# Kernel optimization log

Hardware: AMD Instinct MI355X
Metric: run time of the kernel (lower is better)

The kernel has to match this reference:

```python
import jax, jax.numpy as jnp
import numpy as np

B, T, V, H = 256, 512, 64, 256
IN = 2 * V + 1  # values + masks + delta_t = 129


def setup_inputs() -> dict:
    key = jax.random.key(0)
    ks = jax.random.split(key, 8)
    # sorted positive times with some entries zeroed (ragged padding -> t_exist False)
    t = jnp.sort(jax.random.uniform(ks[0], (B, T)), axis=1)
    keep = jax.random.uniform(ks[1], (B, T)) < 0.9
    times_in = jnp.where(keep, t, 0.0).astype(jnp.float32)
    data_in = jax.random.normal(ks[2], (B, T, V), dtype=jnp.float32)
    mask_in = (jax.random.uniform(ks[3], (B, T, V)) < 0.8).astype(jnp.float32)
    s = 1.0 / np.sqrt(H).astype(np.float32)
    W_ih = jax.random.uniform(ks[4], (3 * H, IN), minval=-s, maxval=s, dtype=jnp.float32)
    W_hh = jax.random.uniform(ks[5], (3 * H, H), minval=-s, maxval=s, dtype=jnp.float32)
    b_ih = jax.random.uniform(ks[6], (3 * H,), minval=-s, maxval=s, dtype=jnp.float32)
    b_hh = jax.random.uniform(ks[7], (3 * H,), minval=-s, maxval=s, dtype=jnp.float32)
    return {"times_in": times_in, "data_in": data_in, "mask_in": mask_in,
            "W_ih": W_ih, "W_hh": W_hh, "b_ih": b_ih, "b_hh": b_hh}


def reference(times_in, data_in, mask_in, W_ih, W_hh, b_ih, b_hh):
    b = times_in.shape[0]
    # delta_ts: times[:,1:] - times[:,:-1], padded with zero at the end
    delta = jnp.concatenate(
        [times_in[:, 1:] - times_in[:, :-1],
         jnp.zeros((b, 1), times_in.dtype)], axis=1)  # [B,T]
    # input_series = cat(values, masks, delta_t) -> [B,T,2V+1]
    x = jnp.concatenate([data_in, mask_in, delta[..., None]], axis=-1)
    t_exist = times_in > 0  # [B,T]
    h0 = jnp.zeros((b, W_hh.shape[1]), x.dtype)

    xs = (jnp.swapaxes(x, 0, 1), jnp.swapaxes(t_exist, 0, 1))  # time-major

    def step(h, inp):
        xt, m = inp  # xt: [B,IN], m: [B]
        gx = xt @ W_ih.T + b_ih  # [B,3H]
        gh = h @ W_hh.T + b_hh   # [B,3H]
        xr, xz, xn = jnp.split(gx, 3, axis=-1)
        hr, hz, hn = jnp.split(gh, 3, axis=-1)
        r = jax.nn.sigmoid(xr + hr)
        z = jax.nn.sigmoid(xz + hz)
        n = jnp.tanh(xn + r * hn)
        h_new = (1.0 - z) * n + z * h
        h = jnp.where(m[:, None], h_new, h)  # masked state carry
        return h, None

    h_final, _ = jax.lax.scan(step, h0, xs)
    return h_final
```

## Files before the change

kernel.cpp:

```cpp
#include <hip/hip_runtime.h>

#define Bn 256
#define Tn 512
#define Vn 64
#define Hn 256
#define INn 129
#define Cc 8
#define NCH (Tn / Cc)
#define WU 68
#define WSZ (768 * WU)
#define GX_OFF (262144)
#define GX_BYTES ((size_t)Bn * Tn * 768 * 2)
#define AST 168
#define CST 264

typedef __fp16 half2_t __attribute__((ext_vector_type(2)));
typedef __fp16 half8_t __attribute__((ext_vector_type(8)));
typedef float f32x4 __attribute__((ext_vector_type(4)));

static __device__ __forceinline__ unsigned int cvt2(float a, float b) {
  return __builtin_bit_cast(unsigned int, __builtin_amdgcn_cvt_pkrtz(a, b));
}

static __device__ __forceinline__ float dot2(unsigned int w, unsigned int x, float acc) {
#if __has_builtin(__builtin_amdgcn_fdot2)
  return __builtin_amdgcn_fdot2(__builtin_bit_cast(half2_t, w),
                                __builtin_bit_cast(half2_t, x), acc, false);
#else
  half2_t a = __builtin_bit_cast(half2_t, w);
  half2_t b = __builtin_bit_cast(half2_t, x);
  return acc + (float)a.x * (float)b.x + (float)a.y * (float)b.y;
#endif
}

static __device__ __forceinline__ float pair_sum(float v) {
#if __has_builtin(__builtin_amdgcn_update_dpp)
  int x = __builtin_amdgcn_update_dpp(0, __builtin_bit_cast(int, v), 0xB1, 0xF, 0xF, true);
  return v + __builtin_bit_cast(float, x);
#else
  int j = __builtin_amdgcn_ds_swizzle(__builtin_bit_cast(int, v), 0x041F);
  return v + __builtin_bit_cast(float, j);
#endif
}

static __device__ __forceinline__ float fast_exp2(float x) {
#if __has_builtin(__builtin_amdgcn_exp2f)
  return __builtin_amdgcn_exp2f(x);
#else
  return exp2f(x);
#endif
}
static __device__ __forceinline__ float fast_rcp(float x) {
#if __has_builtin(__builtin_amdgcn_rcpf)
  return __builtin_amdgcn_rcpf(x);
#else
  return 1.f / x;
#endif
}
static __device__ __forceinline__ float sigmoid_f(float x) {
  return fast_rcp(1.f + fast_exp2(-1.44269504f * x));
}
static __device__ __forceinline__ float tanh_f(float x) {
  return 1.f - 2.f * fast_rcp(1.f + fast_exp2(2.88539008f * x));
}
static __device__ __forceinline__ float h2f(unsigned short u) {
  return (float)__builtin_bit_cast(__fp16, u);
}

__global__ void convert_wih(const float* __restrict__ W_ih, unsigned int* __restrict__ w16) {
  int idx = blockIdx.x * 256 + threadIdx.x;
  if (idx >= WSZ) return;
  int j = idx / WU, c = idx - j * WU;
  int col = 2 * c;
  float f0 = (col < INn) ? W_ih[(size_t)j * INn + col] : 0.f;
  float f1 = (col + 1 < INn) ? W_ih[(size_t)j * INn + col + 1] : 0.f;
  w16[idx] = cvt2(f0, f1);
}

__global__ __launch_bounds__(256, 2)
void gx_gemm(const float* __restrict__ times_in, const float* __restrict__ data_in,
             const float* __restrict__ mask_in, const unsigned int* __restrict__ w16,
             const float* __restrict__ b_ih, const float* __restrict__ b_hh,
             __fp16* __restrict__ gx) {
  __shared__ __align__(16) __fp16 xa[64 * AST];
  __shared__ __align__(16) __fp16 ct[64 * CST];

  const int tid = threadIdx.x;
  const int bt = blockIdx.x;
  const int b = bt >> 3, tc = bt & 7;
  const int t0 = tc * 64;

  {
    int r = tid >> 2, s = tid & 3;
    const float* src = (s < 2)
        ? data_in + ((size_t)b * Tn + t0 + r) * Vn + s * 32
        : mask_in + ((size_t)b * Tn + t0 + r) * Vn + (s - 2) * 32;
    unsigned int* dst = (unsigned int*)(xa + r * AST) + s * 16;
#pragma unroll
    for (int i = 0; i < 8; ++i) {
      float4 v = ((const float4*)src)[i];
      dst[2 * i] = cvt2(v.x, v.y);
      dst[2 * i + 1] = cvt2(v.z, v.w);
    }
  }
  if (tid < 64) {
    int g = t0 + tid;
    float tcur = times_in[(size_t)b * Tn + g];
    float d = (g < Tn - 1) ? times_in[(size_t)b * Tn + g + 1] - tcur : 0.f;
    unsigned int* p = (unsigned int*)(xa + tid * AST + 128);
    p[0] = cvt2(d, 0.f);
#pragma unroll
    for (int i = 1; i < 20; ++i) p[i] = 0u;
  }
  __syncthreads();

  const int w = tid >> 6, lane = tid & 63;
  const int m = lane & 15, q = lane >> 4;

#pragma unroll 1
  for (int nb = 0; nb < 3; ++nb) {
    const int n0 = nb * 256;
    const int nw = n0 + w * 64;

    f32x4 acc[4][4];
#pragma unroll
    for (int i = 0; i < 4; ++i)
#pragma unroll
      for (int j = 0; j < 4; ++j) acc[i][j] = f32x4{0.f, 0.f, 0.f, 0.f};

#pragma unroll
    for (int kt = 0; kt < 5; ++kt) {
      const int k0 = kt * 32 + q * 8;
      half8_t bf[4], af[4];
#pragma unroll
      for (int nt = 0; nt < 4; ++nt) {
        int n = nw + nt * 16 + m;
        uint4 bv = *(const uint4*)(w16 + (size_t)n * WU + (k0 >> 1));
        bf[nt] = __builtin_bit_cast(half8_t, bv);
      }
#pragma unroll
      for (int mt = 0; mt < 4; ++mt) {
        uint4 av = *(const uint4*)(xa + (mt * 16 + m) * AST + k0);
        af[mt] = __builtin_bit_cast(half8_t, av);
      }
#pragma unroll
      for (int mt = 0; mt < 4; ++mt)
#pragma unroll
        for (int nt = 0; nt < 4; ++nt)
          acc[mt][nt] = __builtin_amdgcn_mfma_f32_16x16x32_f16(af[mt], bf[nt], acc[mt][nt], 0, 0, 0);
    }

    float bias[4];
#pragma unroll
    for (int nt = 0; nt < 4; ++nt) {
      int n = nw + nt * 16 + m;
      bias[nt] = b_ih[n] + ((n < 512) ? b_hh[n] : 0.f);
    }

#pragma unroll
    for (int mt = 0; mt < 4; ++mt)
#pragma unroll
      for (int nt = 0; nt < 4; ++nt)
#pragma unroll
        for (int r = 0; r < 4; ++r)
          ct[(mt * 16 + q * 4 + r) * CST + w * 64 + nt * 16 + m] =
              (__fp16)(acc[mt][nt][r] + bias[nt]);
    __syncthreads();

    {
      const int tt = tid >> 2, qq = tid & 3;
      const uint4* src = (const uint4*)(ct + tt * CST) + qq * 8;
      uint4* dst = (uint4*)(gx + ((size_t)b * Tn + t0 + tt) * 768 + n0) + qq * 8;
#pragma unroll
      for (int i = 0; i < 8; ++i) dst[i] = src[i];
    }
    __syncthreads();
  }
}

struct G6 {
  unsigned short r0, r1, z0, z1, n0, n1;
};
static __device__ __forceinline__ G6 load_gx(const unsigned short* p) {
  G6 g;
  g.r0 = p[0];
  g.r1 = p[16];
  g.z0 = p[256];
  g.z1 = p[272];
  g.n0 = p[512];
  g.n1 = p[528];
  return g;
}

__global__ __launch_bounds__(512, 1)
void gru_scan_m1(const float* __restrict__ times_in, const float* __restrict__ W_hh,
                 const float* __restrict__ b_hh, const __fp16* __restrict__ gx,
                 float* __restrict__ out) {
  __shared__ __align__(16) __fp16 hl[2 * Hn];
  __shared__ short act[Tn];
  __shared__ int wave_cnt[8];
  __shared__ int nact_s;

  const int tid = threadIdx.x;
  const int b = blockIdx.x;
  const int lane = tid & 63;
  const int w = tid >> 6;
  const int m = lane & 15;
  const int q = lane >> 4;
  const int d0 = w * 32 + m;

  {
    float tv = times_in[(size_t)b * Tn + tid];
    bool on = tv > 0.f;
    unsigned long long mask = __ballot(on);
    int within = __popcll(mask & ((1ull << lane) - 1ull));
    if (lane == 0) wave_cnt[w] = __popcll(mask);
    __syncthreads();
    int off = 0;
#pragma unroll
    for (int i = 0; i < 8; ++i) off += (i < w) ? wave_cnt[i] : 0;
    if (on) act[off + within] = (short)tid;
    if (tid == 0) {
      int n = 0;
#pragma unroll
      for (int i = 0; i < 8; ++i) n += wave_cnt[i];
      nact_s = n;
    }
  }

  half8_t wb[6][8];
#pragma unroll
  for (int g = 0; g < 3; ++g)
#pragma unroll
    for (int hf = 0; hf < 2; ++hf) {
      const float* wr = W_hh + (size_t)(g * 256 + w * 32 + hf * 16 + m) * Hn;
#pragma unroll
      for (int kc = 0; kc < 8; ++kc) {
        const float4 a = *(const float4*)(wr + kc * 32 + q * 8);
        const float4 c = *(const float4*)(wr + kc * 32 + q * 8 + 4);
        uint4 u;
        u.x = cvt2(a.x, a.y);
        u.y = cvt2(a.z, a.w);
        u.z = cvt2(c.x, c.y);
        u.w = cvt2(c.z, c.w);
        wb[g * 2 + hf][kc] = __builtin_bit_cast(half8_t, u);
      }
    }
  const float bhn0 = b_hh[512 + d0];
  const float bhn1 = b_hh[512 + d0 + 16];

  hl[tid] = (__fp16)0.f;
  __syncthreads();

  const int nact = nact_s;
  const unsigned short* gxs = (const unsigned short*)(gx + (size_t)b * Tn * 768) + d0;

  float h0 = 0.f, h1 = 0.f;
  int cur = 0;

  auto step = [&](G6 g) {
    const uint4* ha = (const uint4*)(hl + cur * Hn);
    uint4 afu[8];
#pragma unroll
    for (int kc = 0; kc < 8; ++kc) afu[kc] = ha[kc * 4 + q];

    f32x4 acc[6];
#pragma unroll
    for (int t = 0; t < 6; ++t) acc[t] = f32x4{0.f, 0.f, 0.f, 0.f};
#pragma unroll
    for (int kc = 0; kc < 8; ++kc) {
      half8_t a = __builtin_bit_cast(half8_t, afu[kc]);
#pragma unroll
      for (int t = 0; t < 6; ++t)
        acc[t] = __builtin_amdgcn_mfma_f32_16x16x32_f16(a, wb[t][kc], acc[t], 0, 0, 0);
    }

    float r0 = sigmoid_f(h2f(g.r0) + acc[0][0]);
    float r1 = sigmoid_f(h2f(g.r1) + acc[1][0]);
    float z0 = sigmoid_f(h2f(g.z0) + acc[2][0]);
    float z1 = sigmoid_f(h2f(g.z1) + acc[3][0]);
    float n0 = tanh_f(h2f(g.n0) + r0 * (acc[4][0] + bhn0));
    float n1 = tanh_f(h2f(g.n1) + r1 * (acc[5][0] + bhn1));
    h0 = z0 * (h0 - n0) + n0;
    h1 = z1 * (h1 - n1) + n1;

    if (q == 0) {
      hl[(cur ^ 1) * Hn + d0] = (__fp16)h0;
      hl[(cur ^ 1) * Hn + d0 + 16] = (__fp16)h1;
    }
    asm volatile("s_waitcnt lgkmcnt(0)" ::: "memory");
    __builtin_amdgcn_s_barrier();
    __builtin_amdgcn_sched_barrier(0);
    cur ^= 1;
  };

  if (nact > 0) {
    G6 ga = load_gx(gxs + (size_t)act[0] * 768);
    G6 gb = load_gx(gxs + (size_t)act[(nact > 1) ? 1 : 0] * 768);
    int i = 0;
#pragma unroll 1
    for (; i + 2 <= nact; i += 2) {
      const int iA = (i + 2 < nact) ? i + 2 : nact - 1;
      const int iB = (i + 3 < nact) ? i + 3 : nact - 1;
      const int tA = act[iA];
      const int tB = act[iB];
      step(ga);
      ga = load_gx(gxs + (size_t)tA * 768);
      step(gb);
      gb = load_gx(gxs + (size_t)tB * 768);
    }
    if (i < nact) step(ga);
  }

  if (q == 0) {
    out[(size_t)b * Hn + d0] = h0;
    out[(size_t)b * Hn + d0 + 16] = h1;
  }
}

template <bool USE_WS>
static __device__ __forceinline__ void phaseA_pass(int col, const unsigned int* __restrict__ w16,
                                                   const float* __restrict__ W_ih,
                                                   const unsigned int* x_lds, float* a) {
  const uint4* wp = (const uint4*)(w16) + (size_t)col * (WU / 4);
  const float* wf = W_ih + (size_t)col * INn;
#pragma unroll 2
  for (int kp = 0; kp < 8; ++kp) {
    uint4 wa, wb;
    if constexpr (USE_WS) {
      wa = wp[2 * kp];
      wb = wp[2 * kp + 1];
    } else {
      const float* f = wf + 16 * kp;
      wa.x = cvt2(f[0], f[1]);   wa.y = cvt2(f[2], f[3]);
      wa.z = cvt2(f[4], f[5]);   wa.w = cvt2(f[6], f[7]);
      wb.x = cvt2(f[8], f[9]);   wb.y = cvt2(f[10], f[11]);
      wb.z = cvt2(f[12], f[13]); wb.w = cvt2(f[14], f[15]);
    }
#pragma unroll
    for (int t = 0; t < Cc; ++t) {
      const uint4* xp = (const uint4*)&x_lds[t * WU + kp * 8];
      uint4 xa = xp[0], xb = xp[1];
      a[t] = dot2(wa.x, xa.x, a[t]);
      a[t] = dot2(wa.y, xa.y, a[t]);
      a[t] = dot2(wa.z, xa.z, a[t]);
      a[t] = dot2(wa.w, xa.w, a[t]);
      a[t] = dot2(wb.x, xb.x, a[t]);
      a[t] = dot2(wb.y, xb.y, a[t]);
      a[t] = dot2(wb.z, xb.z, a[t]);
      a[t] = dot2(wb.w, xb.w, a[t]);
    }
  }
  uint4 wt;
  if constexpr (USE_WS) {
    wt = wp[16];
  } else {
    wt.x = cvt2(wf[128], 0.f); wt.y = 0u; wt.z = 0u; wt.w = 0u;
  }
#pragma unroll
  for (int t = 0; t < Cc; ++t) {
    uint4 xt = *(const uint4*)&x_lds[t * WU + 64];
    a[t] = dot2(wt.x, xt.x, a[t]);
    a[t] = dot2(wt.y, xt.y, a[t]);
  }
}

template <bool USE_WS>
__global__ __launch_bounds__(512, 2)
void gru_scan_fb(const float* __restrict__ times_in, const float* __restrict__ data_in,
                 const float* __restrict__ mask_in, const unsigned int* __restrict__ w16,
                 const float* __restrict__ W_ih, const float* __restrict__ W_hh,
                 const float* __restrict__ b_ih, const float* __restrict__ b_hh,
                 float* __restrict__ out) {
  __shared__ __align__(16) float gx_lds[Cc * 768];
  __shared__ __align__(16) unsigned int x_lds[Cc * WU];
  __shared__ __align__(16) __fp16 h_buf[2 * Hn];
  __shared__ __align__(16) float t_lds[Tn];

  const int tid = threadIdx.x;
  const int b = blockIdx.x;
  const int jg = tid >> 1;
  const int ks = tid & 1;

  t_lds[tid] = times_in[(size_t)b * Tn + tid];

  unsigned int whr[64], whz[64], whn[64];
  {
    const float* w0 = W_hh + (size_t)jg * Hn + ks * 128;
    const float* w1 = W_hh + (size_t)(jg + 256) * Hn + ks * 128;
    const float* w2 = W_hh + (size_t)(jg + 512) * Hn + ks * 128;
#pragma unroll
    for (int c = 0; c < 64; ++c) {
      whr[c] = cvt2(w0[2 * c], w0[2 * c + 1]);
      whz[c] = cvt2(w1[2 * c], w1[2 * c + 1]);
      whn[c] = cvt2(w2[2 * c], w2[2 * c + 1]);
    }
  }
  const float brh = b_hh[jg];
  const float bzh = b_hh[jg + 256];
  const float bhn = b_hh[jg + 512];
  const float bi1 = b_ih[tid];
  const float bi2 = (tid < 256) ? b_ih[512 + tid] : 0.f;

  h_buf[tid] = (__fp16)0.f;
  __syncthreads();

  float hcur = 0.f;
  int cur = 0;
#pragma unroll 1
  for (int ch = 0; ch < NCH; ++ch) {
    const int t0 = ch * Cc;
    {
      int t = tid >> 6;
      int c = tid & 63;
      const float* src = (c < 32)
          ? data_in + ((size_t)b * Tn + t0 + t) * Vn + 2 * c
          : mask_in + ((size_t)b * Tn + t0 + t) * Vn + 2 * (c - 32);
      float2 v = *(const float2*)src;
      x_lds[t * WU + c] = cvt2(v.x, v.y);
      if (tid < Cc) {
        int g = t0 + tid;
        float d = (g < Tn - 1) ? (t_lds[g + 1] - t_lds[g]) : 0.f;
        uint4 tl;
        tl.x = cvt2(d, 0.f); tl.y = 0u; tl.z = 0u; tl.w = 0u;
        *(uint4*)&x_lds[tid * WU + 64] = tl;
      }
    }
    __syncthreads();
    {
      float a[Cc];
#pragma unroll
      for (int t = 0; t < Cc; ++t) a[t] = bi1;
      phaseA_pass<USE_WS>(tid, w16, W_ih, x_lds, a);
#pragma unroll
      for (int t = 0; t < Cc; ++t) gx_lds[t * 768 + tid] = a[t];
      if (tid < 256) {
#pragma unroll
        for (int t = 0; t < Cc; ++t) a[t] = bi2;
        phaseA_pass<USE_WS>(512 + tid, w16, W_ih, x_lds, a);
#pragma unroll
        for (int t = 0; t < Cc; ++t) gx_lds[t * 768 + 512 + tid] = a[t];
      }
    }
    __syncthreads();
    for (int tt = 0; tt < Cc; ++tt) {
      float sr = 0.f, sz = 0.f, shn = 0.f;
      const uint4* hb = (const uint4*)(h_buf + cur * Hn + ks * 128);
#pragma unroll
      for (int c = 0; c < 16; ++c) {
        uint4 hv = hb[c];
        sr = dot2(whr[4 * c + 0], hv.x, sr);
        sz = dot2(whz[4 * c + 0], hv.x, sz);
        shn = dot2(whn[4 * c + 0], hv.x, shn);
        sr = dot2(whr[4 * c + 1], hv.y, sr);
        sz = dot2(whz[4 * c + 1], hv.y, sz);
        shn = dot2(whn[4 * c + 1], hv.y, shn);
        sr = dot2(whr[4 * c + 2], hv.z, sr);
        sz = dot2(whz[4 * c + 2], hv.z, sz);
        shn = dot2(whn[4 * c + 2], hv.z, shn);
        sr = dot2(whr[4 * c + 3], hv.w, sr);
        sz = dot2(whz[4 * c + 3], hv.w, sz);
        shn = dot2(whn[4 * c + 3], hv.w, shn);
      }
      float gxr = gx_lds[tt * 768 + jg];
      float gxz = gx_lds[tt * 768 + 256 + jg];
      float gxn = gx_lds[tt * 768 + 512 + jg];
      sr = pair_sum(sr);
      sz = pair_sum(sz);
      shn = pair_sum(shn);
      float r = sigmoid_f(gxr + sr + brh);
      float z = sigmoid_f(gxz + sz + bzh);
      float n = tanh_f(gxn + r * (shn + bhn));
      float hN = (1.f - z) * n + z * hcur;
      hcur = (t_lds[t0 + tt] > 0.f) ? hN : hcur;
      if (ks == 0) h_buf[(cur ^ 1) * Hn + jg] = (__fp16)hcur;
      __syncthreads();
      cur ^= 1;
    }
  }
  if (ks == 0) out[(size_t)b * Hn + jg] = hcur;
}

extern "C" void kernel_launch(void* const* d_in, const int* in_sizes, int n_in,
                              void* d_out, int out_size, void* d_ws, size_t ws_size,
                              hipStream_t stream) {
  const float* times_in = (const float*)d_in[0];
  const float* data_in = (const float*)d_in[1];
  const float* mask_in = (const float*)d_in[2];
  const float* W_ih = (const float*)d_in[3];
  const float* W_hh = (const float*)d_in[4];
  const float* b_ih = (const float*)d_in[5];
  const float* b_hh = (const float*)d_in[6];
  float* out = (float*)d_out;

  unsigned int* w16 = (unsigned int*)d_ws;
  __fp16* gx = (__fp16*)((char*)d_ws + GX_OFF);

  if (ws_size >= GX_OFF + GX_BYTES) {
    hipLaunchKernelGGL(convert_wih, dim3((WSZ + 255) / 256), dim3(256), 0, stream, W_ih, w16);
    hipLaunchKernelGGL(gx_gemm, dim3(2048), dim3(256), 0, stream,
                       times_in, data_in, mask_in, w16, b_ih, b_hh, gx);
    hipLaunchKernelGGL(gru_scan_m1, dim3(Bn), dim3(512), 0, stream,
                       times_in, W_hh, b_hh, gx, out);
  } else if (ws_size >= (size_t)WSZ * 4) {
    hipLaunchKernelGGL(convert_wih, dim3((WSZ + 255) / 256), dim3(256), 0, stream, W_ih, w16);
    hipLaunchKernelGGL((gru_scan_fb<true>), dim3(Bn), dim3(512), 0, stream,
                       times_in, data_in, mask_in, w16, W_ih, W_hh, b_ih, b_hh, out);
  } else {
    hipLaunchKernelGGL((gru_scan_fb<false>), dim3(Bn), dim3(512), 0, stream,
                       times_in, data_in, mask_in, (const unsigned int*)nullptr, W_ih, W_hh,
                       b_ih, b_hh, out);
  }
}
```

Measured before the change: 703.6 us.

## Split GRU scan: MFMA for r/z gates, per-thread dot2 for n gate

The per-step recurrent matvec is split. The r and z gates stay on MFMA with four accumulators per wave, while the n-gate rows are held as packed fp16 weights in registers and computed with scalar dot2 instructions, with each pair of threads splitting the K dimension. The aim is to shorten the MFMA dependency chain on the serial critical path and to spread the gate math over all 512 threads instead of one quarter of the lanes. In exchange it adds a 64-register weight array per thread, cross-lane shuffles and a pair reduction, which may raise register pressure and per-step latency.

```diff
diff --git a/kernel.cpp b/kernel.cpp
--- a/kernel.cpp
+++ b/kernel.cpp
@@ -178,22 +178,8 @@
   }
 }
 
-struct G6 {
-  unsigned short r0, r1, z0, z1, n0, n1;
-};
-static __device__ __forceinline__ G6 load_gx(const unsigned short* p) {
-  G6 g;
-  g.r0 = p[0];
-  g.r1 = p[16];
-  g.z0 = p[256];
-  g.z1 = p[272];
-  g.n0 = p[512];
-  g.n1 = p[528];
-  return g;
-}
-
 __global__ __launch_bounds__(512, 1)
-void gru_scan_m1(const float* __restrict__ times_in, const float* __restrict__ W_hh,
+void gru_scan_h4(const float* __restrict__ times_in, const float* __restrict__ W_hh,
                  const float* __restrict__ b_hh, const __fp16* __restrict__ gx,
                  float* __restrict__ out) {
   __shared__ __align__(16) __fp16 hl[2 * Hn];
@@ -207,7 +193,8 @@
   const int w = tid >> 6;
   const int m = lane & 15;
   const int q = lane >> 4;
-  const int d0 = w * 32 + m;
+  const int jg = tid >> 1;
+  const int ks = tid & 1;
 
   {
     float tv = times_in[(size_t)b * Tn + tid];
@@ -228,9 +215,9 @@
     }
   }
 
-  half8_t wb[6][8];
-#pragma unroll
-  for (int g = 0; g < 3; ++g)
+  half8_t wb[4][8];
+#pragma unroll
+  for (int g = 0; g < 2; ++g)
 #pragma unroll
     for (int hf = 0; hf < 2; ++hf) {
       const float* wr = W_hh + (size_t)(g * 256 + w * 32 + hf * 16 + m) * Hn;
@@ -246,76 +233,90 @@
         wb[g * 2 + hf][kc] = __builtin_bit_cast(half8_t, u);
       }
     }
-  const float bhn0 = b_hh[512 + d0];
-  const float bhn1 = b_hh[512 + d0 + 16];
+
+  unsigned int whn[64];
+  {
+    const float* w2 = W_hh + (size_t)(jg + 512) * Hn + ks * 128;
+#pragma unroll
+    for (int c = 0; c < 64; ++c) whn[c] = cvt2(w2[2 * c], w2[2 * c + 1]);
+  }
+  const float bhn = b_hh[jg + 512];
 
   hl[tid] = (__fp16)0.f;
   __syncthreads();
 
   const int nact = nact_s;
-  const unsigned short* gxs = (const unsigned short*)(gx + (size_t)b * Tn * 768) + d0;
-
-  float h0 = 0.f, h1 = 0.f;
+  const __fp16* gxb = gx + (size_t)b * Tn * 768;
+  float hcur = 0.f;
   int cur = 0;
 
-  auto step = [&](G6 g) {
-    const uint4* ha = (const uint4*)(hl + cur * Hn);
-    uint4 afu[8];
-#pragma unroll
-    for (int kc = 0; kc < 8; ++kc) afu[kc] = ha[kc * 4 + q];
-
-    f32x4 acc[6];
-#pragma unroll
-    for (int t = 0; t < 6; ++t) acc[t] = f32x4{0.f, 0.f, 0.f, 0.f};
-#pragma unroll
-    for (int kc = 0; kc < 8; ++kc) {
-      half8_t a = __builtin_bit_cast(half8_t, afu[kc]);
-#pragma unroll
-      for (int t = 0; t < 6; ++t)
-        acc[t] = __builtin_amdgcn_mfma_f32_16x16x32_f16(a, wb[t][kc], acc[t], 0, 0, 0);
-    }
-
-    float r0 = sigmoid_f(h2f(g.r0) + acc[0][0]);
-    float r1 = sigmoid_f(h2f(g.r1) + acc[1][0]);
-    float z0 = sigmoid_f(h2f(g.z0) + acc[2][0]);
-    float z1 = sigmoid_f(h2f(g.z1) + acc[3][0]);
-    float n0 = tanh_f(h2f(g.n0) + r0 * (acc[4][0] + bhn0));
-    float n1 = tanh_f(h2f(g.n1) + r1 * (acc[5][0] + bhn1));
-    h0 = z0 * (h0 - n0) + n0;
-    h1 = z1 * (h1 - n1) + n1;
-
-    if (q == 0) {
-      hl[(cur ^ 1) * Hn + d0] = (__fp16)h0;
-      hl[(cur ^ 1) * Hn + d0 + 16] = (__fp16)h1;
-    }
-    asm volatile("s_waitcnt lgkmcnt(0)" ::: "memory");
-    __builtin_amdgcn_s_barrier();
-    __builtin_amdgcn_sched_barrier(0);
-    cur ^= 1;
-  };
-
   if (nact > 0) {
-    G6 ga = load_gx(gxs + (size_t)act[0] * 768);
-    G6 gb = load_gx(gxs + (size_t)act[(nact > 1) ? 1 : 0] * 768);
-    int i = 0;
+    int t0i = act[0];
+    float gr = (float)gxb[(size_t)t0i * 768 + jg];
+    float gz = (float)gxb[(size_t)t0i * 768 + 256 + jg];
+    float gn = (float)gxb[(size_t)t0i * 768 + 512 + jg];
+
 #pragma unroll 1
-    for (; i + 2 <= nact; i += 2) {
-      const int iA = (i + 2 < nact) ? i + 2 : nact - 1;
-      const int iB = (i + 3 < nact) ? i + 3 : nact - 1;
-      const int tA = act[iA];
-      const int tB = act[iB];
-      step(ga);
-      ga = load_gx(gxs + (size_t)tA * 768);
-      step(gb);
-      gb = load_gx(gxs + (size_t)tB * 768);
-    }
-    if (i < nact) step(ga);
-  }
-
-  if (q == 0) {
-    out[(size_t)b * Hn + d0] = h0;
-    out[(size_t)b * Hn + d0 + 16] = h1;
-  }
+    for (int i = 0; i < nact; ++i) {
+      const int ni = (i + 1 < nact) ? (i + 1) : (nact - 1);
+      const int tnx = act[ni];
+      const __fp16* p = gxb + (size_t)tnx * 768;
+      __fp16 pr = p[jg], pz = p[256 + jg], pn = p[512 + jg];
+
+      const uint4* ha = (const uint4*)(hl + cur * Hn);
+      uint4 afu[8];
+#pragma unroll
+      for (int kc = 0; kc < 8; ++kc) afu[kc] = ha[kc * 4 + q];
+
+      f32x4 aR0 = f32x4{0.f, 0.f, 0.f, 0.f};
+      f32x4 aR1 = f32x4{0.f, 0.f, 0.f, 0.f};
+      f32x4 aZ0 = f32x4{0.f, 0.f, 0.f, 0.f};
+      f32x4 aZ1 = f32x4{0.f, 0.f, 0.f, 0.f};
+#pragma unroll
+      for (int kc = 0; kc < 8; ++kc) {
+        half8_t a = __builtin_bit_cast(half8_t, afu[kc]);
+        aR0 = __builtin_amdgcn_mfma_f32_16x16x32_f16(a, wb[0][kc], aR0, 0, 0, 0);
+        aR1 = __builtin_amdgcn_mfma_f32_16x16x32_f16(a, wb[1][kc], aR1, 0, 0, 0);
+        aZ0 = __builtin_amdgcn_mfma_f32_16x16x32_f16(a, wb[2][kc], aZ0, 0, 0, 0);
+        aZ1 = __builtin_amdgcn_mfma_f32_16x16x32_f16(a, wb[3][kc], aZ1, 0, 0, 0);
+      }
+
+      const uint4* hb = (const uint4*)(hl + cur * Hn) + ks * 16;
+      float s0 = 0.f, s1 = 0.f, s2 = 0.f, s3 = 0.f;
+#pragma unroll
+      for (int c = 0; c < 16; ++c) {
+        uint4 hv = hb[c];
+        s0 = dot2(whn[4 * c + 0], hv.x, s0);
+        s1 = dot2(whn[4 * c + 1], hv.y, s1);
+        s2 = dot2(whn[4 * c + 2], hv.z, s2);
+        s3 = dot2(whn[4 * c + 3], hv.w, s3);
+      }
+      float shn = pair_sum((s0 + s1) + (s2 + s3));
+
+      const int src = (lane >> 1) & 15;
+      float r0v = __shfl(aR0[0], src, 64);
+      float r1v = __shfl(aR1[0], src, 64);
+      float z0v = __shfl(aZ0[0], src, 64);
+      float z1v = __shfl(aZ1[0], src, 64);
+      float rp = (lane & 32) ? r1v : r0v;
+      float zp = (lane & 32) ? z1v : z0v;
+
+      float r = sigmoid_f(gr + rp);
+      float z = sigmoid_f(gz + zp);
+      float n = tanh_f(gn + r * (shn + bhn));
+      hcur = (1.f - z) * n + z * hcur;
+
+      if (ks == 0) hl[(cur ^ 1) * Hn + jg] = (__fp16)hcur;
+      asm volatile("s_waitcnt lgkmcnt(0)" ::: "memory");
+      __builtin_amdgcn_s_barrier();
+      __builtin_amdgcn_sched_barrier(0);
+      cur ^= 1;
+
+      gr = (float)pr; gz = (float)pz; gn = (float)pn;
+    }
+  }
+
+  if (ks == 0) out[(size_t)b * Hn + jg] = hcur;
 }
 
 template <bool USE_WS>
@@ -500,7 +501,7 @@
     hipLaunchKernelGGL(convert_wih, dim3((WSZ + 255) / 256), dim3(256), 0, stream, W_ih, w16);
     hipLaunchKernelGGL(gx_gemm, dim3(2048), dim3(256), 0, stream,
                        times_in, data_in, mask_in, w16, b_ih, b_hh, gx);
-    hipLaunchKernelGGL(gru_scan_m1, dim3(Bn), dim3(512), 0, stream,
+    hipLaunchKernelGGL(gru_scan_h4, dim3(Bn), dim3(512), 0, stream,
                        times_in, W_hh, b_hh, gx, out);
   } else if (ws_size >= (size_t)WSZ * 4) {
     hipLaunchKernelGGL(convert_wih, dim3((WSZ + 255) / 256), dim3(256), 0, stream, W_ih, w16);
```

Result: slower. 844.1 us (+20.0%).
